# Optimization experiments

Measured on AMD Instinct MI355X. Metric: run time of the kernel, lower is better.

The kernel has to match this reference:

```python
import jax, jax.numpy as jnp
import numpy as np

OFFSET_SCALE = 6.0
H = W = 256


def setup_inputs() -> dict:
    key = jax.random.key(0)
    k1, k2, k3, k4 = jax.random.split(key, 4)
    B = 128
    Offset = jax.random.normal(k1, (B, 3, H, W), dtype=jnp.float32) * 0.05
    Posmap_kpt = jax.random.normal(k2, (B, 3, H, W), dtype=jnp.float32)
    mean_posmap = jax.random.normal(k3, (3, H, W), dtype=jnp.float32)
    uv_kpt = jax.random.randint(k4, (68, 2), 0, H)
    return {"Offset": Offset, "Posmap_kpt": Posmap_kpt,
            "mean_posmap": mean_posmap, "uv_kpt": uv_kpt}


def _safe_norm(d):
    # row-wise L2 norm with zero-safe gradient (row 0 of d is exactly zero)
    sq = jnp.sum(d * d, axis=1)
    pos = sq > 0
    return jnp.where(pos, jnp.sqrt(jnp.where(pos, sq, 1.0)), 0.0)


def _kabsch(src, dst):
    # src, dst: [68, 3] -> similarity transform (scaled R [3,3], t [3])
    s1 = jnp.sum(_safe_norm(src - src[0]))
    s2 = jnp.sum(_safe_norm(dst - dst[0]))
    scale = s2 / s1
    A = src * scale
    AA = A - A.mean(axis=0)
    BB = dst - dst.mean(axis=0)
    Hm = AA.T @ BB                        # [3,3] cross-covariance
    U, S, Vh = jnp.linalg.svd(Hm, full_matrices=False)
    R = Vh.T @ U.T                        # torch.svd returns V, so R = V U^T
    t = jnp.mean(dst - A @ R.T, axis=0)
    return R * scale, t


def reference(Offset, Posmap_kpt, mean_posmap, uv_kpt):
    B = Offset.shape[0]
    offsetmap = (Offset * OFFSET_SCALE + mean_posmap).transpose(0, 2, 3, 1)  # [B,H,W,3]
    kptmap = Posmap_kpt.transpose(0, 2, 3, 1)                                # [B,H,W,3]
    kpt_dst = kptmap[:, uv_kpt[:, 0], uv_kpt[:, 1]]                          # [B,68,3]
    kpt_src = offsetmap[:, uv_kpt[:, 0], uv_kpt[:, 1]]                       # [B,68,3]
    offsetflat = offsetmap.reshape(B, H * W, 3)                              # [B,65536,3]
    R, t = jax.vmap(_kabsch)(kpt_src, kpt_dst)                               # [B,3,3], [B,3]
    outpos = jnp.einsum('bnd,bed->bne', offsetflat, R) + t[:, None, :]       # x @ R^T + t
    return outpos.reshape(B, H, W, 3).transpose(0, 3, 1, 2)
```

## Files before the change

kernel.cpp:

```cpp
#include <hip/hip_runtime.h>

#define HW (256*256)
#define NKPT 68
#define NB 128

__device__ inline void inv3x3(const double m[9], double inv[9], double* detOut) {
    double c00 =  m[4]*m[8] - m[5]*m[7];
    double c01 = -(m[3]*m[8] - m[5]*m[6]);
    double c02 =  m[3]*m[7] - m[4]*m[6];
    double det = m[0]*c00 + m[1]*c01 + m[2]*c02;
    double id = 1.0 / det;
    inv[0] = c00 * id;
    inv[1] = (m[2]*m[7] - m[1]*m[8]) * id;
    inv[2] = (m[1]*m[5] - m[2]*m[4]) * id;
    inv[3] = c01 * id;
    inv[4] = (m[0]*m[8] - m[2]*m[6]) * id;
    inv[5] = (m[2]*m[3] - m[0]*m[5]) * id;
    inv[6] = c02 * id;
    inv[7] = (m[1]*m[6] - m[0]*m[7]) * id;
    inv[8] = (m[0]*m[4] - m[1]*m[3]) * id;
    *detOut = det;
}

__global__ __launch_bounds__(128) void kabsch_kernel(
    const float* __restrict__ Offset,
    const float* __restrict__ Posmap,
    const float* __restrict__ meanp,
    const int*   __restrict__ uv,
    float* __restrict__ RT)
{
    const int b   = blockIdx.x;
    const int tid = threadIdx.x;
    __shared__ double red[17][NKPT];
    __shared__ double res[17];

    if (tid < NKPT) {
        const int r  = uv[2*tid],   c  = uv[2*tid+1];
        const int r0 = uv[0],       c0 = uv[1];
        const int p  = r  * 256 + c;
        const int p0 = r0 * 256 + c0;
        const float* offB = Offset + (size_t)b * 3 * HW;
        const float* posB = Posmap + (size_t)b * 3 * HW;
        double s[3], d[3], s0[3], d0[3];
        #pragma unroll
        for (int k = 0; k < 3; ++k) {
            s[k]  = (double)offB[k*HW + p ] * 6.0 + (double)meanp[k*HW + p ];
            d[k]  = (double)posB[k*HW + p ];
            s0[k] = (double)offB[k*HW + p0] * 6.0 + (double)meanp[k*HW + p0];
            d0[k] = (double)posB[k*HW + p0];
        }
        int q = 0;
        #pragma unroll
        for (int k = 0; k < 3; ++k) red[q++][tid] = s[k];
        #pragma unroll
        for (int k = 0; k < 3; ++k) red[q++][tid] = d[k];
        #pragma unroll
        for (int i = 0; i < 3; ++i)
            #pragma unroll
            for (int j = 0; j < 3; ++j) red[q++][tid] = s[i] * d[j];
        double ns2 = 0.0, nd2 = 0.0;
        #pragma unroll
        for (int k = 0; k < 3; ++k) {
            double e = s[k] - s0[k]; ns2 += e*e;
            double f = d[k] - d0[k]; nd2 += f*f;
        }
        red[q++][tid] = (ns2 > 0.0) ? sqrt(ns2) : 0.0;
        red[q++][tid] = (nd2 > 0.0) ? sqrt(nd2) : 0.0;
    }
    __syncthreads();
    if (tid < 17) {
        double acc = 0.0;
        for (int i = 0; i < NKPT; ++i) acc += red[tid][i];
        res[tid] = acc;
    }
    __syncthreads();
    if (tid == 0) {
        const double sumS[3] = {res[0], res[1], res[2]};
        const double sumD[3] = {res[3], res[4], res[5]};
        double cross[9];
        #pragma unroll
        for (int k = 0; k < 9; ++k) cross[k] = res[6+k];
        const double s1 = res[15], s2 = res[16];
        const double scale = s2 / s1;
        double mS[3], mD[3];
        #pragma unroll
        for (int k = 0; k < 3; ++k) { mS[k] = sumS[k] / NKPT; mD[k] = sumD[k] / NKPT; }
        double Wm[9];
        #pragma unroll
        for (int i = 0; i < 3; ++i)
            #pragma unroll
            for (int j = 0; j < 3; ++j)
                Wm[i*3+j] = scale * (cross[i*3+j] - (double)NKPT * mS[i] * mD[j]);
        for (int it = 0; it < 20; ++it) {
            double inv[9], det;
            inv3x3(Wm, inv, &det);
            double g  = cbrt(fabs(det));
            double gi = 1.0 / g;
            double Wn[9];
            #pragma unroll
            for (int r = 0; r < 3; ++r)
                #pragma unroll
                for (int c = 0; c < 3; ++c)
                    Wn[r*3+c] = 0.5 * (gi * Wm[r*3+c] + g * inv[c*3+r]);
            #pragma unroll
            for (int k = 0; k < 9; ++k) Wm[k] = Wn[k];
        }
        float* o = RT + b * 12;
        #pragma unroll
        for (int e = 0; e < 3; ++e)
            #pragma unroll
            for (int d = 0; d < 3; ++d)
                o[e*3+d] = (float)(scale * Wm[d*3+e]);
        #pragma unroll
        for (int e = 0; e < 3; ++e) {
            double acc = mD[e];
            #pragma unroll
            for (int d = 0; d < 3; ++d) acc -= scale * mS[d] * Wm[d*3+e];
            o[9+e] = (float)acc;
        }
    }
}

__global__ __launch_bounds__(256) void apply_kernel(
    const float* __restrict__ Offset,
    const float* __restrict__ meanp,
    const float* __restrict__ RT,
    float* __restrict__ out)
{
    const int blk   = blockIdx.x;
    const int b     = blk >> 6;
    const int chunk = blk & 63;
    const int p     = chunk * 1024 + threadIdx.x * 4;

    const float* rt = RT + b * 12;
    const float r00 = rt[0], r01 = rt[1], r02 = rt[2];
    const float r10 = rt[3], r11 = rt[4], r12 = rt[5];
    const float r20 = rt[6], r21 = rt[7], r22 = rt[8];
    const float t0  = rt[9], t1  = rt[10], t2 = rt[11];

    const size_t base = (size_t)b * 3 * HW + p;
    const float4 a0 = *(const float4*)(Offset + base + 0*HW);
    const float4 a1 = *(const float4*)(Offset + base + 1*HW);
    const float4 a2 = *(const float4*)(Offset + base + 2*HW);
    const float4 m0 = *(const float4*)(meanp + p + 0*HW);
    const float4 m1 = *(const float4*)(meanp + p + 1*HW);
    const float4 m2 = *(const float4*)(meanp + p + 2*HW);

    float4 o0, o1, o2;
    {
        float x, y, z;
        #define DO_LANE(L) \
            x = fmaf(6.0f, a0.L, m0.L); \
            y = fmaf(6.0f, a1.L, m1.L); \
            z = fmaf(6.0f, a2.L, m2.L); \
            o0.L = fmaf(r00, x, fmaf(r01, y, fmaf(r02, z, t0))); \
            o1.L = fmaf(r10, x, fmaf(r11, y, fmaf(r12, z, t1))); \
            o2.L = fmaf(r20, x, fmaf(r21, y, fmaf(r22, z, t2)));
        DO_LANE(x) DO_LANE(y) DO_LANE(z) DO_LANE(w)
        #undef DO_LANE
    }
    *(float4*)(out + base + 0*HW) = o0;
    *(float4*)(out + base + 1*HW) = o1;
    *(float4*)(out + base + 2*HW) = o2;
}

extern "C" void kernel_launch(void* const* d_in, const int* in_sizes, int n_in,
                              void* d_out, int out_size, void* d_ws, size_t ws_size,
                              hipStream_t stream) {
    const float* Offset = (const float*)d_in[0];
    const float* Posmap = (const float*)d_in[1];
    const float* meanp  = (const float*)d_in[2];
    const int*   uv     = (const int*)d_in[3];
    float* out = (float*)d_out;
    float* RT  = (float*)d_ws;

    kabsch_kernel<<<NB, 128, 0, stream>>>(Offset, Posmap, meanp, uv, RT);
    apply_kernel<<<NB * 64, 256, 0, stream>>>(Offset, meanp, RT, out);
}
```

Before: 228.0 us.

## Process four float4 groups per thread with nontemporal I/O and fewer polar iterations

The apply kernel now has each thread handle four float4 groups per channel. All Offset and mean loads are issued up front, and Offset reads and output writes use nontemporal builtins, with a quarter as many blocks. The aim is more memory-level parallelism and less cache pollution from streamed data that is never reused. The polar-decomposition Newton iteration in the Kabsch kernel drops from 20 to 8 steps, which shortens the serial single-thread tail but risks a less converged rotation on poorly conditioned inputs.

```diff
diff --git a/kernel.cpp b/kernel.cpp
--- a/kernel.cpp
+++ b/kernel.cpp
@@ -3,6 +3,8 @@
 #define HW (256*256)
 #define NKPT 68
 #define NB 128
+
+typedef float v4f __attribute__((ext_vector_type(4)));
 
 __device__ inline void inv3x3(const double m[9], double inv[9], double* detOut) {
     double c00 =  m[4]*m[8] - m[5]*m[7];
@@ -91,7 +93,7 @@
             #pragma unroll
             for (int j = 0; j < 3; ++j)
                 Wm[i*3+j] = scale * (cross[i*3+j] - (double)NKPT * mS[i] * mD[j]);
-        for (int it = 0; it < 20; ++it) {
+        for (int it = 0; it < 8; ++it) {
             double inv[9], det;
             inv3x3(Wm, inv, &det);
             double g  = cbrt(fabs(det));
@@ -127,10 +129,10 @@
     const float* __restrict__ RT,
     float* __restrict__ out)
 {
-    const int blk   = blockIdx.x;
-    const int b     = blk >> 6;
-    const int chunk = blk & 63;
-    const int p     = chunk * 1024 + threadIdx.x * 4;
+    const int blk  = blockIdx.x;
+    const int b    = blk >> 4;
+    const int slab = blk & 15;
+    const int p0   = slab * 4096 + threadIdx.x * 4;
 
     const float* rt = RT + b * 12;
     const float r00 = rt[0], r01 = rt[1], r02 = rt[2];
@@ -138,30 +140,41 @@
     const float r20 = rt[6], r21 = rt[7], r22 = rt[8];
     const float t0  = rt[9], t1  = rt[10], t2 = rt[11];
 
-    const size_t base = (size_t)b * 3 * HW + p;
-    const float4 a0 = *(const float4*)(Offset + base + 0*HW);
-    const float4 a1 = *(const float4*)(Offset + base + 1*HW);
-    const float4 a2 = *(const float4*)(Offset + base + 2*HW);
-    const float4 m0 = *(const float4*)(meanp + p + 0*HW);
-    const float4 m1 = *(const float4*)(meanp + p + 1*HW);
-    const float4 m2 = *(const float4*)(meanp + p + 2*HW);
+    const size_t bbase = (size_t)b * 3 * HW;
 
-    float4 o0, o1, o2;
-    {
-        float x, y, z;
-        #define DO_LANE(L) \
-            x = fmaf(6.0f, a0.L, m0.L); \
-            y = fmaf(6.0f, a1.L, m1.L); \
-            z = fmaf(6.0f, a2.L, m2.L); \
-            o0.L = fmaf(r00, x, fmaf(r01, y, fmaf(r02, z, t0))); \
-            o1.L = fmaf(r10, x, fmaf(r11, y, fmaf(r12, z, t1))); \
-            o2.L = fmaf(r20, x, fmaf(r21, y, fmaf(r22, z, t2)));
-        DO_LANE(x) DO_LANE(y) DO_LANE(z) DO_LANE(w)
-        #undef DO_LANE
+    v4f a[3][4], m[3][4];
+    #pragma unroll
+    for (int g = 0; g < 4; ++g) {
+        const int p = p0 + g * 1024;
+        #pragma unroll
+        for (int ch = 0; ch < 3; ++ch)
+            a[ch][g] = __builtin_nontemporal_load((const v4f*)(Offset + bbase + (size_t)ch * HW + p));
     }
-    *(float4*)(out + base + 0*HW) = o0;
-    *(float4*)(out + base + 1*HW) = o1;
-    *(float4*)(out + base + 2*HW) = o2;
+    #pragma unroll
+    for (int g = 0; g < 4; ++g) {
+        const int p = p0 + g * 1024;
+        #pragma unroll
+        for (int ch = 0; ch < 3; ++ch)
+            m[ch][g] = *(const v4f*)(meanp + (size_t)ch * HW + p);
+    }
+
+    #pragma unroll
+    for (int g = 0; g < 4; ++g) {
+        const int p = p0 + g * 1024;
+        v4f o0, o1, o2;
+        #pragma unroll
+        for (int L = 0; L < 4; ++L) {
+            float x = fmaf(6.0f, a[0][g][L], m[0][g][L]);
+            float y = fmaf(6.0f, a[1][g][L], m[1][g][L]);
+            float z = fmaf(6.0f, a[2][g][L], m[2][g][L]);
+            o0[L] = fmaf(r00, x, fmaf(r01, y, fmaf(r02, z, t0)));
+            o1[L] = fmaf(r10, x, fmaf(r11, y, fmaf(r12, z, t1)));
+            o2[L] = fmaf(r20, x, fmaf(r21, y, fmaf(r22, z, t2)));
+        }
+        __builtin_nontemporal_store(o0, (v4f*)(out + bbase + 0*HW + p));
+        __builtin_nontemporal_store(o1, (v4f*)(out + bbase + 1*HW + p));
+        __builtin_nontemporal_store(o2, (v4f*)(out + bbase + 2*HW + p));
+    }
 }
 
 extern "C" void kernel_launch(void* const* d_in, const int* in_sizes, int n_in,
@@ -175,5 +188,5 @@
     float* RT  = (float*)d_ws;
 
     kabsch_kernel<<<NB, 128, 0, stream>>>(Offset, Posmap, meanp, uv, RT);
-    apply_kernel<<<NB * 64, 256, 0, stream>>>(Offset, meanp, RT, out);
+    apply_kernel<<<NB * 16, 256, 0, stream>>>(Offset, meanp, RT, out);
 }
```

Result: no change. 227.0 us (-0.5%).
